# Performance work log

Measured on AMD Instinct MI355X. Metric: run time of the kernel, lower is better.

The kernel has to match this reference:

```python
import jax, jax.numpy as jnp
import numpy as np

B, D, E, K, H, C = 8192, 1024, 8, 2, 2048, 512
LN_EPS = 1e-5


def setup_inputs() -> dict:
    key = jax.random.key(0)
    ks = jax.random.split(key, 6)
    s = 0.02
    return {
        "x": jax.random.normal(ks[0], (B, D), dtype=jnp.float32),
        "Wr": jax.random.normal(ks[1], (E, D), dtype=jnp.float32) * s,  # router weight [E,D]
        "br": jnp.zeros((E,), dtype=jnp.float32),
        "gamma": jnp.ones((E, D), dtype=jnp.float32),   # per-expert LayerNorm scale
        "beta": jnp.zeros((E, D), dtype=jnp.float32),   # per-expert LayerNorm shift
        "W1": jax.random.normal(ks[2], (E, H, D), dtype=jnp.float32) * s,
        "b1": jnp.zeros((E, H), dtype=jnp.float32),
        "W2": jax.random.normal(ks[3], (E, C, H), dtype=jnp.float32) * s,
        "b2": jnp.zeros((E, C), dtype=jnp.float32),
    }


def reference(x, Wr, br, gamma, beta, W1, b1, W2, b2):
    # Router + top-k gating (softmax over the k selected logits only)
    router_logits = x @ Wr.T + br                       # [B,E]
    topk_vals, topk_idx = jax.lax.top_k(router_logits, K)  # [B,K]
    topk_w = jax.nn.softmax(topk_vals, axis=-1)         # [B,K]
    # Dense gate [B,E]: gate[b,e] = sum_j topk_w[b,j] * (topk_idx[b,j]==e)
    gate = (jax.nn.one_hot(topk_idx, E, dtype=x.dtype) * topk_w[..., None]).sum(axis=1)

    # LayerNorm statistics are expert-independent; affine is per-expert
    mu = x.mean(axis=-1, keepdims=True)
    var = ((x - mu) ** 2).mean(axis=-1, keepdims=True)
    xn = (x - mu) * jax.lax.rsqrt(var + LN_EPS)          # [B,D]

    out = jnp.zeros((x.shape[0], C), dtype=x.dtype)
    for e in range(E):  # small fixed expert count
        xe = xn * gamma[e] + beta[e]                     # [B,D]
        h = jax.nn.gelu(xe @ W1[e].T + b1[e], approximate=False)  # [B,H]
        y = h @ W2[e].T + b2[e]                          # [B,C]
        out = out + gate[:, e:e + 1] * y
    return out
```

## Files before the change

### kernel.cpp

```cpp
#include <hip/hip_runtime.h>
#include <hip/hip_bf16.h>
#include <math.h>

#define B_TOK 8192
#define DDIM 1024
#define NEXP 8
#define HDIM 2048
#define CDIM 512
#define LN_EPS 1e-5f
#define MAXTILES 136
#define MAXROWS (MAXTILES * 128)

typedef __attribute__((ext_vector_type(4))) float f32x4;
typedef __attribute__((ext_vector_type(8))) short bf16x8;

__device__ __forceinline__ unsigned short f2bf(float f) {
  __hip_bfloat16 h = __float2bfloat16(f);
  return *reinterpret_cast<unsigned short*>(&h);
}
__device__ __forceinline__ float bf2f(unsigned short u) {
  unsigned int x = ((unsigned int)u) << 16;
  return *reinterpret_cast<float*>(&x);
}

__device__ __forceinline__ void gload_lds16(const unsigned short* g, unsigned short* l) {
  __builtin_amdgcn_global_load_lds(
      (const __attribute__((address_space(1))) unsigned int*)g,
      (__attribute__((address_space(3))) unsigned int*)l, 16, 0, 0);
}

__global__ __launch_bounds__(256) void router_ln_kernel(
    const float* __restrict__ x, const float* __restrict__ Wr,
    const float* __restrict__ br, int* __restrict__ eidx,
    float* __restrict__ wgt, unsigned short* __restrict__ xn) {
  const int wid = threadIdx.x >> 6;
  const int lane = threadIdx.x & 63;
  const int tok = blockIdx.x * 4 + wid;

  const float4* xr = reinterpret_cast<const float4*>(x + (size_t)tok * DDIM);
  float4 xv[4];
  float sum = 0.f, sumsq = 0.f;
  float dot[NEXP];
#pragma unroll
  for (int e = 0; e < NEXP; ++e) dot[e] = 0.f;

#pragma unroll
  for (int i = 0; i < 4; ++i) {
    const int f = i * 64 + lane;
    float4 v = xr[f];
    xv[i] = v;
    sum += v.x + v.y + v.z + v.w;
    sumsq += v.x * v.x + v.y * v.y + v.z * v.z + v.w * v.w;
#pragma unroll
    for (int e = 0; e < NEXP; ++e) {
      float4 w = reinterpret_cast<const float4*>(Wr + e * DDIM)[f];
      dot[e] += v.x * w.x + v.y * w.y + v.z * w.z + v.w * w.w;
    }
  }
#pragma unroll
  for (int off = 32; off > 0; off >>= 1) {
    sum += __shfl_xor(sum, off);
    sumsq += __shfl_xor(sumsq, off);
#pragma unroll
    for (int e = 0; e < NEXP; ++e) dot[e] += __shfl_xor(dot[e], off);
  }
  const float mu = sum * (1.f / DDIM);
  const float var = sumsq * (1.f / DDIM) - mu * mu;
  const float rs = rsqrtf(var + LN_EPS);

  float lg[NEXP];
#pragma unroll
  for (int e = 0; e < NEXP; ++e) lg[e] = dot[e] + br[e];

  int i1 = 0; float v1 = lg[0];
#pragma unroll
  for (int e = 1; e < NEXP; ++e) { if (lg[e] > v1) { v1 = lg[e]; i1 = e; } }
  int i2 = -1; float v2 = -3.4e38f;
#pragma unroll
  for (int e = 0; e < NEXP; ++e) { if (e != i1 && lg[e] > v2) { v2 = lg[e]; i2 = e; } }

  const float e2 = __expf(v2 - v1);
  const float inv = 1.f / (1.f + e2);
  if (lane == 0) {
    eidx[tok * 2] = i1; eidx[tok * 2 + 1] = i2;
    wgt[tok * 2] = inv; wgt[tok * 2 + 1] = e2 * inv;
  }

  unsigned short* xnr = xn + (size_t)tok * DDIM;
#pragma unroll
  for (int i = 0; i < 4; ++i) {
    const int f = i * 64 + lane;
    float4 v = xv[i];
    ushort4 o;
    o.x = f2bf((v.x - mu) * rs);
    o.y = f2bf((v.y - mu) * rs);
    o.z = f2bf((v.z - mu) * rs);
    o.w = f2bf((v.w - mu) * rs);
    reinterpret_cast<ushort4*>(xnr)[f] = o;
  }
}

__global__ __launch_bounds__(256) void sort_kernel(
    const int* __restrict__ eidx,
    int* __restrict__ tokRow,
    int* __restrict__ slot2row,
    int* __restrict__ tileExp,
    int* __restrict__ nTilesOut) {
  __shared__ int cnt[NEXP], segBase[NEXP], cur[NEXP];
  const int tid = threadIdx.x;
  if (tid < NEXP) { cnt[tid] = 0; cur[tid] = 0; }
  __syncthreads();
  for (int t = tid; t < B_TOK * 2; t += 256)
    atomicAdd(&cnt[eidx[t]], 1);
  __syncthreads();
  if (tid == 0) {
    int c = 0;
    for (int e = 0; e < NEXP; ++e) {
      segBase[e] = c;
      const int nt = (cnt[e] + 127) >> 7;
      for (int t = 0; t < nt; ++t) tileExp[(c >> 7) + t] = e;
      for (int p = c + cnt[e]; p < c + nt * 128; ++p) tokRow[p] = 0;
      c += nt * 128;
    }
    *nTilesOut = c >> 7;
  }
  __syncthreads();
  for (int t = tid; t < B_TOK * 2; t += 256) {
    const int e = eidx[t];
    const int pos = segBase[e] + atomicAdd(&cur[e], 1);
    tokRow[pos] = t >> 1;
    slot2row[t] = pos;
  }
}

__global__ __launch_bounds__(256) void prep_w1_kernel(
    const float* __restrict__ W1, const float* __restrict__ gamma,
    const float* __restrict__ beta, const float* __restrict__ b1,
    unsigned short* __restrict__ W1g, float* __restrict__ c1) {
  const int eh = blockIdx.x;
  const int e = eh >> 11;
  const int tid = threadIdx.x;

  float4 w = reinterpret_cast<const float4*>(W1 + (size_t)eh * DDIM)[tid];
  float4 g = reinterpret_cast<const float4*>(gamma + (size_t)e * DDIM)[tid];
  float4 bt = reinterpret_cast<const float4*>(beta + (size_t)e * DDIM)[tid];

  ushort4 o;
  o.x = f2bf(w.x * g.x); o.y = f2bf(w.y * g.y);
  o.z = f2bf(w.z * g.z); o.w = f2bf(w.w * g.w);
  reinterpret_cast<ushort4*>(W1g + (size_t)eh * DDIM)[tid] = o;

  float p = w.x * bt.x + w.y * bt.y + w.z * bt.z + w.w * bt.w;
#pragma unroll
  for (int off = 32; off > 0; off >>= 1) p += __shfl_xor(p, off);
  __shared__ float red[4];
  const int lane = tid & 63, wv = tid >> 6;
  if (lane == 0) red[wv] = p;
  __syncthreads();
  if (tid == 0) c1[eh] = b1[eh] + red[0] + red[1] + red[2] + red[3];
}

__global__ __launch_bounds__(256) void prep_w2_kernel(
    const float* __restrict__ W2, unsigned short* __restrict__ W2b) {
  const int idx = blockIdx.x * 256 + threadIdx.x;
  float4 w = reinterpret_cast<const float4*>(W2)[idx];
  ushort4 o;
  o.x = f2bf(w.x); o.y = f2bf(w.y); o.z = f2bf(w.z); o.w = f2bf(w.w);
  reinterpret_cast<ushort4*>(W2b)[idx] = o;
}

#define BM 128
#define BN 128
#define BKK 64

__global__ __launch_bounds__(256) void gemm1_gelu_kernel(
    const unsigned short* __restrict__ A,
    const unsigned short* __restrict__ W1g,
    const float* __restrict__ c1,
    const int* __restrict__ tokRow, const int* __restrict__ tileExp,
    const int* __restrict__ nTiles,
    unsigned short* __restrict__ Hout) {
  const int bx = blockIdx.x, by = blockIdx.y;
  if (bx >= *nTiles) return;
  const int e = tileExp[bx];

  __shared__ unsigned short lA[BM * BKK];
  __shared__ unsigned short lB[BN * BKK];
  const int tid = threadIdx.x;
  const int lane = tid & 63;
  const int wid = tid >> 6;
  const int wr = wid >> 1, wc = wid & 1;

  const unsigned short* Bbase = W1g + ((size_t)e * HDIM + (size_t)by * BN) * DDIM;
  const float* bias = c1 + e * HDIM;

  const int r = tid >> 3;
  const int cc = (tid & 7) * 8;
  int aRow[4];
#pragma unroll
  for (int i = 0; i < 4; ++i) aRow[i] = tokRow[bx * BM + i * 32 + r];

  f32x4 acc[4][4];
#pragma unroll
  for (int m = 0; m < 4; ++m)
#pragma unroll
    for (int n = 0; n < 4; ++n)
#pragma unroll
      for (int j = 0; j < 4; ++j) acc[m][n][j] = 0.f;

  for (int k0 = 0; k0 < DDIM; k0 += BKK) {
#pragma unroll
    for (int i = 0; i < 4; ++i)
      gload_lds16(A + (size_t)aRow[i] * DDIM + k0 + cc,
                  &lA[(i * 32 + r) * BKK + cc]);
#pragma unroll
    for (int i = 0; i < 4; ++i)
      gload_lds16(Bbase + (size_t)(i * 32 + r) * DDIM + k0 + cc,
                  &lB[(i * 32 + r) * BKK + cc]);
    __syncthreads();
#pragma unroll
    for (int kk = 0; kk < 2; ++kk) {
      bf16x8 af[4], bfr[4];
      const int kof = kk * 32 + (lane >> 4) * 8;
#pragma unroll
      for (int m = 0; m < 4; ++m)
        af[m] = *reinterpret_cast<const bf16x8*>(
            &lA[(wr * 64 + m * 16 + (lane & 15)) * BKK + kof]);
#pragma unroll
      for (int n = 0; n < 4; ++n)
        bfr[n] = *reinterpret_cast<const bf16x8*>(
            &lB[(wc * 64 + n * 16 + (lane & 15)) * BKK + kof]);
#pragma unroll
      for (int m = 0; m < 4; ++m)
#pragma unroll
        for (int n = 0; n < 4; ++n)
          acc[m][n] = __builtin_amdgcn_mfma_f32_16x16x32_bf16(af[m], bfr[n], acc[m][n], 0, 0, 0);
    }
    __syncthreads();
  }

  const int row0 = bx * BM + wr * 64;
  const int col0 = by * BN + wc * 64;
#pragma unroll
  for (int n = 0; n < 4; ++n) {
    const int col = col0 + n * 16 + (lane & 15);
    const float bv = bias[col];
#pragma unroll
    for (int m = 0; m < 4; ++m) {
#pragma unroll
      for (int j = 0; j < 4; ++j) {
        const int row = row0 + m * 16 + (lane >> 4) * 4 + j;
        const float v = acc[m][n][j] + bv;
        const float gl = 0.5f * v * (1.f + erff(v * 0.70710678118654752f));
        Hout[(size_t)row * HDIM + col] = f2bf(gl);
      }
    }
  }
}

__global__ __launch_bounds__(256) void gemm2_kernel(
    const unsigned short* __restrict__ Hbuf,
    const unsigned short* __restrict__ W2b,
    const int* __restrict__ tileExp, const int* __restrict__ nTiles,
    unsigned short* __restrict__ Y) {
  const int bx = blockIdx.x, by = blockIdx.y;
  if (bx >= *nTiles) return;
  const int e = tileExp[bx];

  __shared__ unsigned short lA[BM * BKK];
  __shared__ unsigned short lB[BN * BKK];
  const int tid = threadIdx.x;
  const int lane = tid & 63;
  const int wid = tid >> 6;
  const int wr = wid >> 1, wc = wid & 1;

  const unsigned short* Abase = Hbuf + (size_t)bx * BM * HDIM;
  const unsigned short* Bbase = W2b + ((size_t)e * CDIM + (size_t)by * BN) * HDIM;

  f32x4 acc[4][4];
#pragma unroll
  for (int m = 0; m < 4; ++m)
#pragma unroll
    for (int n = 0; n < 4; ++n)
#pragma unroll
      for (int j = 0; j < 4; ++j) acc[m][n][j] = 0.f;

  const int r = tid >> 3;
  const int cc = (tid & 7) * 8;

  for (int k0 = 0; k0 < HDIM; k0 += BKK) {
#pragma unroll
    for (int i = 0; i < 4; ++i)
      gload_lds16(Abase + (size_t)(i * 32 + r) * HDIM + k0 + cc,
                  &lA[(i * 32 + r) * BKK + cc]);
#pragma unroll
    for (int i = 0; i < 4; ++i)
      gload_lds16(Bbase + (size_t)(i * 32 + r) * HDIM + k0 + cc,
                  &lB[(i * 32 + r) * BKK + cc]);
    __syncthreads();
#pragma unroll
    for (int kk = 0; kk < 2; ++kk) {
      bf16x8 af[4], bfr[4];
      const int kof = kk * 32 + (lane >> 4) * 8;
#pragma unroll
      for (int m = 0; m < 4; ++m)
        af[m] = *reinterpret_cast<const bf16x8*>(
            &lA[(wr * 64 + m * 16 + (lane & 15)) * BKK + kof]);
#pragma unroll
      for (int n = 0; n < 4; ++n)
        bfr[n] = *reinterpret_cast<const bf16x8*>(
            &lB[(wc * 64 + n * 16 + (lane & 15)) * BKK + kof]);
#pragma unroll
      for (int m = 0; m < 4; ++m)
#pragma unroll
        for (int n = 0; n < 4; ++n)
          acc[m][n] = __builtin_amdgcn_mfma_f32_16x16x32_bf16(af[m], bfr[n], acc[m][n], 0, 0, 0);
    }
    __syncthreads();
  }

  const int row0 = bx * BM + wr * 64;
  const int col0 = by * BN + wc * 64;
#pragma unroll
  for (int m = 0; m < 4; ++m) {
#pragma unroll
    for (int j = 0; j < 4; ++j) {
      const int row = row0 + m * 16 + (lane >> 4) * 4 + j;
#pragma unroll
      for (int n = 0; n < 4; ++n) {
        const int col = col0 + n * 16 + (lane & 15);
        Y[(size_t)row * CDIM + col] = f2bf(acc[m][n][j]);
      }
    }
  }
}

__global__ __launch_bounds__(256) void combine_kernel(
    const unsigned short* __restrict__ Y, const int* __restrict__ slot2row,
    const int* __restrict__ eidx, const float* __restrict__ wgt,
    const float* __restrict__ b2, float* __restrict__ out) {
  const int idx = blockIdx.x * 256 + threadIdx.x;
  const int b = idx >> 7;
  const int c4 = (idx & 127) * 4;
  const int r0 = slot2row[b * 2], r1 = slot2row[b * 2 + 1];
  const int e0 = eidx[b * 2], e1 = eidx[b * 2 + 1];
  const float w0 = wgt[b * 2], w1 = wgt[b * 2 + 1];
  ushort4 y0 = *reinterpret_cast<const ushort4*>(Y + (size_t)r0 * CDIM + c4);
  ushort4 y1 = *reinterpret_cast<const ushort4*>(Y + (size_t)r1 * CDIM + c4);
  float4 bb0 = *reinterpret_cast<const float4*>(b2 + e0 * CDIM + c4);
  float4 bb1 = *reinterpret_cast<const float4*>(b2 + e1 * CDIM + c4);
  float4 o;
  o.x = w0 * (bf2f(y0.x) + bb0.x) + w1 * (bf2f(y1.x) + bb1.x);
  o.y = w0 * (bf2f(y0.y) + bb0.y) + w1 * (bf2f(y1.y) + bb1.y);
  o.z = w0 * (bf2f(y0.z) + bb0.z) + w1 * (bf2f(y1.z) + bb1.z);
  o.w = w0 * (bf2f(y0.w) + bb0.w) + w1 * (bf2f(y1.w) + bb1.w);
  *reinterpret_cast<float4*>(out + (size_t)b * CDIM + c4) = o;
}

extern "C" void kernel_launch(void* const* d_in, const int* in_sizes, int n_in,
                              void* d_out, int out_size, void* d_ws, size_t ws_size,
                              hipStream_t stream) {
  const float* x     = (const float*)d_in[0];
  const float* Wr    = (const float*)d_in[1];
  const float* br    = (const float*)d_in[2];
  const float* gamma = (const float*)d_in[3];
  const float* beta  = (const float*)d_in[4];
  const float* W1    = (const float*)d_in[5];
  const float* b1    = (const float*)d_in[6];
  const float* W2    = (const float*)d_in[7];
  const float* b2    = (const float*)d_in[8];
  float* out = (float*)d_out;

  char* ws = (char*)d_ws;
  unsigned short* xn   = (unsigned short*)(ws);
  unsigned short* hbuf = (unsigned short*)(ws + (size_t)16 * 1048576);
  unsigned short* W1g  = (unsigned short*)(ws + (size_t)84 * 1048576);
  unsigned short* ybuf = (unsigned short*)(ws + (size_t)84 * 1048576);
  unsigned short* W2b  = (unsigned short*)(ws + (size_t)116 * 1048576);
  char* misc           = ws + (size_t)132 * 1048576;
  float* c1      = (float*)(misc);
  int* eidx      = (int*)(misc + 65536);
  float* wgt     = (float*)(misc + 2 * 65536);
  int* slot2row  = (int*)(misc + 3 * 65536);
  int* tokRow    = (int*)(misc + 4 * 65536);
  int* tileExp   = (int*)(misc + 4 * 65536 + 69632);
  int* nTiles    = tileExp + MAXTILES;

  router_ln_kernel<<<dim3(B_TOK / 4), dim3(256), 0, stream>>>(x, Wr, br, eidx, wgt, xn);
  sort_kernel<<<dim3(1), dim3(256), 0, stream>>>(eidx, tokRow, slot2row, tileExp, nTiles);
  prep_w1_kernel<<<dim3(NEXP * HDIM), dim3(256), 0, stream>>>(W1, gamma, beta, b1, W1g, c1);
  prep_w2_kernel<<<dim3((NEXP * CDIM * HDIM / 4) / 256), dim3(256), 0, stream>>>(W2, W2b);

  gemm1_gelu_kernel<<<dim3(MAXTILES, HDIM / BN), dim3(256), 0, stream>>>(
      xn, W1g, c1, tokRow, tileExp, nTiles, hbuf);
  gemm2_kernel<<<dim3(MAXTILES, CDIM / BN), dim3(256), 0, stream>>>(
      hbuf, W2b, tileExp, nTiles, ybuf);
  combine_kernel<<<dim3(B_TOK * CDIM / 4 / 256), dim3(256), 0, stream>>>(
      ybuf, slot2row, eidx, wgt, b2, out);
}
```

Before: 315.4 us.

## Rewrite grouped GEMM1 as 256x256 double-buffered 8-wave kernel with swizzled LDS

Replaces the 128x128 single-buffered GEMM1 with a 512-thread, 256x256-tile kernel. It double-buffers global-to-LDS loads and issues the next stage while MFMAs run, using explicit waitcnt/barrier phases, setprio and an XOR-swizzled LDS layout to avoid bank conflicts. Expert segments are padded to 256 rows, and GEMM2 indexing is adapted to the new tiles. The sort kernel switches to wave-ballot aggregated atomics with parallel padding fill, and W2b reuses the xn buffer after GEMM1. Larger padding adds wasted rows, and the hand-written synchronization risks subtle ordering bugs.

```diff
diff --git a/kernel.cpp b/kernel.cpp
--- a/kernel.cpp
+++ b/kernel.cpp
@@ -8,8 +8,8 @@
 #define HDIM 2048
 #define CDIM 512
 #define LN_EPS 1e-5f
-#define MAXTILES 136
-#define MAXROWS (MAXTILES * 128)
+#define MAXT256 72
+#define MAXROWS (MAXT256 * 256)
 
 typedef __attribute__((ext_vector_type(4))) float f32x4;
 typedef __attribute__((ext_vector_type(8))) short bf16x8;
@@ -106,28 +106,51 @@
     int* __restrict__ slot2row,
     int* __restrict__ tileExp,
     int* __restrict__ nTilesOut) {
-  __shared__ int cnt[NEXP], segBase[NEXP], cur[NEXP];
+  __shared__ int cnt[NEXP], segBase[NEXP], segEnd[NEXP], cur[NEXP];
   const int tid = threadIdx.x;
+  const int lane = tid & 63;
   if (tid < NEXP) { cnt[tid] = 0; cur[tid] = 0; }
   __syncthreads();
-  for (int t = tid; t < B_TOK * 2; t += 256)
-    atomicAdd(&cnt[eidx[t]], 1);
+  for (int t = tid; t < B_TOK * 2; t += 256) {
+    const int e = eidx[t];
+#pragma unroll
+    for (int k = 0; k < NEXP; ++k) {
+      unsigned long long m = __ballot(e == k);
+      if (m && lane == 0) atomicAdd(&cnt[k], __popcll(m));
+    }
+  }
   __syncthreads();
   if (tid == 0) {
     int c = 0;
     for (int e = 0; e < NEXP; ++e) {
       segBase[e] = c;
-      const int nt = (cnt[e] + 127) >> 7;
-      for (int t = 0; t < nt; ++t) tileExp[(c >> 7) + t] = e;
-      for (int p = c + cnt[e]; p < c + nt * 128; ++p) tokRow[p] = 0;
-      c += nt * 128;
-    }
-    *nTilesOut = c >> 7;
+      const int nt = (cnt[e] + 255) >> 8;
+      for (int t = 0; t < nt; ++t) tileExp[(c >> 8) + t] = e;
+      c += nt * 256;
+      segEnd[e] = c;
+    }
+    *nTilesOut = c >> 8;
   }
   __syncthreads();
+  for (int e = 0; e < NEXP; ++e) {
+    const int lo = segBase[e] + cnt[e], hi = segEnd[e];
+    for (int p = lo + tid; p < hi; p += 256) tokRow[p] = 0;
+  }
   for (int t = tid; t < B_TOK * 2; t += 256) {
     const int e = eidx[t];
-    const int pos = segBase[e] + atomicAdd(&cur[e], 1);
+    int pos = 0;
+#pragma unroll
+    for (int k = 0; k < NEXP; ++k) {
+      unsigned long long m = __ballot(e == k);
+      if (m) {
+        const int leader = __ffsll((unsigned long long)m) - 1;
+        int base = 0;
+        if (lane == leader) base = atomicAdd(&cur[k], (int)__popcll(m));
+        base = __shfl(base, leader);
+        if (e == k)
+          pos = segBase[k] + base + (int)__popcll(m & ((1ULL << lane) - 1ULL));
+      }
+    }
     tokRow[pos] = t >> 1;
     slot2row[t] = pos;
   }
@@ -169,11 +192,38 @@
   reinterpret_cast<ushort4*>(W2b)[idx] = o;
 }
 
-#define BM 128
-#define BN 128
-#define BKK 64
-
-__global__ __launch_bounds__(256) void gemm1_gelu_kernel(
+template <int QM, int QN>
+__device__ __forceinline__ void phase16(
+    const unsigned short* ldsA, const unsigned short* ldsB,
+    int wm, int wn, int l15, int l4, int l7, f32x4 (&acc)[8][4]) {
+  bf16x8 af[4][2], bfr[2][2];
+#pragma unroll
+  for (int mm = 0; mm < 4; ++mm)
+#pragma unroll
+    for (int ks = 0; ks < 2; ++ks)
+      af[mm][ks] = *reinterpret_cast<const bf16x8*>(
+          &ldsA[(wm * 128 + QM * 64 + mm * 16 + l15) * 64 + ((ks * 4 + l4) ^ l7) * 8]);
+#pragma unroll
+  for (int nn = 0; nn < 2; ++nn)
+#pragma unroll
+    for (int ks = 0; ks < 2; ++ks)
+      bfr[nn][ks] = *reinterpret_cast<const bf16x8*>(
+          &ldsB[(wn * 64 + QN * 32 + nn * 16 + l15) * 64 + ((ks * 4 + l4) ^ l7) * 8]);
+  asm volatile("s_barrier" ::: "memory");
+  __builtin_amdgcn_s_setprio(1);
+#pragma unroll
+  for (int ks = 0; ks < 2; ++ks)
+#pragma unroll
+    for (int mm = 0; mm < 4; ++mm)
+#pragma unroll
+      for (int nn = 0; nn < 2; ++nn)
+        acc[QM * 4 + mm][QN * 2 + nn] = __builtin_amdgcn_mfma_f32_16x16x32_bf16(
+            af[mm][ks], bfr[nn][ks], acc[QM * 4 + mm][QN * 2 + nn], 0, 0, 0);
+  __builtin_amdgcn_s_setprio(0);
+  asm volatile("s_barrier" ::: "memory");
+}
+
+__global__ __launch_bounds__(512, 2) void gemm1_8p_kernel(
     const unsigned short* __restrict__ A,
     const unsigned short* __restrict__ W1g,
     const float* __restrict__ c1,
@@ -184,79 +234,97 @@
   if (bx >= *nTiles) return;
   const int e = tileExp[bx];
 
-  __shared__ unsigned short lA[BM * BKK];
-  __shared__ unsigned short lB[BN * BKK];
+  __shared__ unsigned short lds[2][2][256 * 64];
+
   const int tid = threadIdx.x;
   const int lane = tid & 63;
   const int wid = tid >> 6;
-  const int wr = wid >> 1, wc = wid & 1;
-
-  const unsigned short* Bbase = W1g + ((size_t)e * HDIM + (size_t)by * BN) * DDIM;
-  const float* bias = c1 + e * HDIM;
-
-  const int r = tid >> 3;
-  const int cc = (tid & 7) * 8;
-  int aRow[4];
-#pragma unroll
-  for (int i = 0; i < 4; ++i) aRow[i] = tokRow[bx * BM + i * 32 + r];
-
-  f32x4 acc[4][4];
-#pragma unroll
-  for (int m = 0; m < 4; ++m)
+  const int wm = wid >> 2;
+  const int wn = wid & 3;
+  const int l15 = lane & 15, l4 = lane >> 4, l7 = lane & 7;
+
+  const unsigned short* Bg = W1g + ((size_t)e * HDIM + (size_t)by * 256) * DDIM;
+
+  int tr[4];
+#pragma unroll
+  for (int i = 0; i < 4; ++i) tr[i] = tokRow[bx * 256 + i * 64 + (tid >> 3)];
+  const int sl8 = ((tid & 7) ^ ((tid >> 3) & 7)) * 8;
+
+  f32x4 acc[8][4];
+#pragma unroll
+  for (int m = 0; m < 8; ++m)
 #pragma unroll
     for (int n = 0; n < 4; ++n)
 #pragma unroll
       for (int j = 0; j < 4; ++j) acc[m][n][j] = 0.f;
 
-  for (int k0 = 0; k0 < DDIM; k0 += BKK) {
-#pragma unroll
-    for (int i = 0; i < 4; ++i)
-      gload_lds16(A + (size_t)aRow[i] * DDIM + k0 + cc,
-                  &lA[(i * 32 + r) * BKK + cc]);
-#pragma unroll
-    for (int i = 0; i < 4; ++i)
-      gload_lds16(Bbase + (size_t)(i * 32 + r) * DDIM + k0 + cc,
-                  &lB[(i * 32 + r) * BKK + cc]);
-    __syncthreads();
-#pragma unroll
-    for (int kk = 0; kk < 2; ++kk) {
-      bf16x8 af[4], bfr[4];
-      const int kof = kk * 32 + (lane >> 4) * 8;
-#pragma unroll
-      for (int m = 0; m < 4; ++m)
-        af[m] = *reinterpret_cast<const bf16x8*>(
-            &lA[(wr * 64 + m * 16 + (lane & 15)) * BKK + kof]);
-#pragma unroll
-      for (int n = 0; n < 4; ++n)
-        bfr[n] = *reinterpret_cast<const bf16x8*>(
-            &lB[(wc * 64 + n * 16 + (lane & 15)) * BKK + kof]);
-#pragma unroll
-      for (int m = 0; m < 4; ++m)
-#pragma unroll
-        for (int n = 0; n < 4; ++n)
-          acc[m][n] = __builtin_amdgcn_mfma_f32_16x16x32_bf16(af[m], bfr[n], acc[m][n], 0, 0, 0);
-    }
-    __syncthreads();
-  }
-
-  const int row0 = bx * BM + wr * 64;
-  const int col0 = by * BN + wc * 64;
-#pragma unroll
-  for (int n = 0; n < 4; ++n) {
-    const int col = col0 + n * 16 + (lane & 15);
-    const float bv = bias[col];
-#pragma unroll
-    for (int m = 0; m < 4; ++m) {
+  auto stage8 = [&](int b, int k0) {
+#pragma unroll
+    for (int h = 0; h < 2; ++h)
+#pragma unroll
+      for (int q = 0; q < 2; ++q)
+        gload_lds16(A + (size_t)tr[h * 2 + q] * DDIM + k0 + sl8,
+                    &lds[b][0][h * 8192 + q * 4096 + tid * 8]);
+#pragma unroll
+    for (int h = 0; h < 2; ++h)
+#pragma unroll
+      for (int q = 0; q < 2; ++q)
+        gload_lds16(Bg + (size_t)(h * 128 + q * 64 + (tid >> 3)) * DDIM + k0 + sl8,
+                    &lds[b][1][h * 8192 + q * 4096 + tid * 8]);
+  };
+
+  stage8(0, 0);
+  stage8(1, 64);
+
+  int cur = 0;
+#pragma unroll 1
+  for (int kt = 0; kt < 15; ++kt) {
+    asm volatile("s_waitcnt vmcnt(8)" ::: "memory");
+    __builtin_amdgcn_sched_barrier(0);
+    asm volatile("s_barrier" ::: "memory");
+    const unsigned short* ldsA = lds[cur][0];
+    const unsigned short* ldsB = lds[cur][1];
+    phase16<0, 0>(ldsA, ldsB, wm, wn, l15, l4, l7, acc);
+    phase16<0, 1>(ldsA, ldsB, wm, wn, l15, l4, l7, acc);
+    phase16<1, 0>(ldsA, ldsB, wm, wn, l15, l4, l7, acc);
+    phase16<1, 1>(ldsA, ldsB, wm, wn, l15, l4, l7, acc);
+    if (kt < 14) stage8(cur, (kt + 2) * 64);
+    cur ^= 1;
+  }
+  asm volatile("s_waitcnt vmcnt(0)" ::: "memory");
+  __builtin_amdgcn_sched_barrier(0);
+  asm volatile("s_barrier" ::: "memory");
+  {
+    const unsigned short* ldsA = lds[cur][0];
+    const unsigned short* ldsB = lds[cur][1];
+    phase16<0, 0>(ldsA, ldsB, wm, wn, l15, l4, l7, acc);
+    phase16<0, 1>(ldsA, ldsB, wm, wn, l15, l4, l7, acc);
+    phase16<1, 0>(ldsA, ldsB, wm, wn, l15, l4, l7, acc);
+    phase16<1, 1>(ldsA, ldsB, wm, wn, l15, l4, l7, acc);
+  }
+
+  const float* biasp = c1 + e * HDIM + by * 256 + wn * 64;
+  unsigned short* Hbase = Hout + (size_t)(bx * 256 + wm * 128) * HDIM + by * 256 + wn * 64;
+#pragma unroll
+  for (int m = 0; m < 8; ++m) {
+#pragma unroll
+    for (int n = 0; n < 4; ++n) {
+      const int col = n * 16 + l15;
+      const float bv = biasp[col];
 #pragma unroll
       for (int j = 0; j < 4; ++j) {
-        const int row = row0 + m * 16 + (lane >> 4) * 4 + j;
+        const int row = m * 16 + l4 * 4 + j;
         const float v = acc[m][n][j] + bv;
         const float gl = 0.5f * v * (1.f + erff(v * 0.70710678118654752f));
-        Hout[(size_t)row * HDIM + col] = f2bf(gl);
+        Hbase[(size_t)row * HDIM + col] = f2bf(gl);
       }
     }
   }
 }
+
+#define BM 128
+#define BN 128
+#define BKK 64
 
 __global__ __launch_bounds__(256) void gemm2_kernel(
     const unsigned short* __restrict__ Hbuf,
@@ -264,8 +332,8 @@
     const int* __restrict__ tileExp, const int* __restrict__ nTiles,
     unsigned short* __restrict__ Y) {
   const int bx = blockIdx.x, by = blockIdx.y;
-  if (bx >= *nTiles) return;
-  const int e = tileExp[bx];
+  if ((bx >> 1) >= *nTiles) return;
+  const int e = tileExp[bx >> 1];
 
   __shared__ unsigned short lA[BM * BKK];
   __shared__ unsigned short lB[BN * BKK];
@@ -373,27 +441,29 @@
 
   char* ws = (char*)d_ws;
   unsigned short* xn   = (unsigned short*)(ws);
+  unsigned short* W2b  = (unsigned short*)(ws);
   unsigned short* hbuf = (unsigned short*)(ws + (size_t)16 * 1048576);
-  unsigned short* W1g  = (unsigned short*)(ws + (size_t)84 * 1048576);
-  unsigned short* ybuf = (unsigned short*)(ws + (size_t)84 * 1048576);
-  unsigned short* W2b  = (unsigned short*)(ws + (size_t)116 * 1048576);
-  char* misc           = ws + (size_t)132 * 1048576;
+  unsigned short* W1g  = (unsigned short*)(ws + (size_t)88 * 1048576);
+  unsigned short* ybuf = (unsigned short*)(ws + (size_t)88 * 1048576);
+  char* misc           = ws + (size_t)120 * 1048576;
   float* c1      = (float*)(misc);
   int* eidx      = (int*)(misc + 65536);
   float* wgt     = (float*)(misc + 2 * 65536);
   int* slot2row  = (int*)(misc + 3 * 65536);
   int* tokRow    = (int*)(misc + 4 * 65536);
-  int* tileExp   = (int*)(misc + 4 * 65536 + 69632);
-  int* nTiles    = tileExp + MAXTILES;
+  int* tileExp   = (int*)(misc + 4 * 65536 + 131072);
+  int* nTiles    = tileExp + MAXT256;
 
   router_ln_kernel<<<dim3(B_TOK / 4), dim3(256), 0, stream>>>(x, Wr, br, eidx, wgt, xn);
   sort_kernel<<<dim3(1), dim3(256), 0, stream>>>(eidx, tokRow, slot2row, tileExp, nTiles);
   prep_w1_kernel<<<dim3(NEXP * HDIM), dim3(256), 0, stream>>>(W1, gamma, beta, b1, W1g, c1);
+
+  gemm1_8p_kernel<<<dim3(MAXT256, HDIM / 256), dim3(512), 0, stream>>>(
+      xn, W1g, c1, tokRow, tileExp, nTiles, hbuf);
+
   prep_w2_kernel<<<dim3((NEXP * CDIM * HDIM / 4) / 256), dim3(256), 0, stream>>>(W2, W2b);
 
-  gemm1_gelu_kernel<<<dim3(MAXTILES, HDIM / BN), dim3(256), 0, stream>>>(
-      xn, W1g, c1, tokRow, tileExp, nTiles, hbuf);
-  gemm2_kernel<<<dim3(MAXTILES, CDIM / BN), dim3(256), 0, stream>>>(
+  gemm2_kernel<<<dim3(MAXT256 * 2, CDIM / BN), dim3(256), 0, stream>>>(
       hbuf, W2b, tileExp, nTiles, ybuf);
   combine_kernel<<<dim3(B_TOK * CDIM / 4 / 256), dim3(256), 0, stream>>>(
       ybuf, slot2row, eidx, wgt, b2, out);
```

After: 411.6 us. 1.3x slower.

## Swizzle LDS tiles, remap grid for XCD locality, pad experts to 256 rows

Applied to the files above, without the earlier changes.

Adds an XOR swizzle to the LDS layout of A and B tiles in both GEMMs so the MFMA fragment reads avoid bank conflicts. Flattens the grid and remaps block indices so that blocks sharing the same weight or activation tiles land on the same XCD (blockIdx & 7), aiming for better L2 reuse. Pads expert segments to 256 rows so each expert covers whole pairs of 128-row tiles. Reorders the workspace so W2b reuses the xn region and is converted after GEMM1. The coarser padding adds more wasted rows per expert.

```diff
diff --git a/kernel.cpp b/kernel.cpp
--- a/kernel.cpp
+++ b/kernel.cpp
@@ -8,8 +8,8 @@
 #define HDIM 2048
 #define CDIM 512
 #define LN_EPS 1e-5f
-#define MAXTILES 136
-#define MAXROWS (MAXTILES * 128)
+#define MAXT256 72
+#define MAXROWS (MAXT256 * 256)
 
 typedef __attribute__((ext_vector_type(4))) float f32x4;
 typedef __attribute__((ext_vector_type(8))) short bf16x8;
@@ -117,12 +117,12 @@
     int c = 0;
     for (int e = 0; e < NEXP; ++e) {
       segBase[e] = c;
-      const int nt = (cnt[e] + 127) >> 7;
-      for (int t = 0; t < nt; ++t) tileExp[(c >> 7) + t] = e;
-      for (int p = c + cnt[e]; p < c + nt * 128; ++p) tokRow[p] = 0;
-      c += nt * 128;
-    }
-    *nTilesOut = c >> 7;
+      const int nt = (cnt[e] + 255) >> 8;
+      for (int t = 0; t < nt; ++t) tileExp[(c >> 8) + t] = e;
+      for (int p = c + cnt[e]; p < c + nt * 256; ++p) tokRow[p] = 0;
+      c += nt * 256;
+    }
+    *nTilesOut = c >> 8;
   }
   __syncthreads();
   for (int t = tid; t < B_TOK * 2; t += 256) {
@@ -180,9 +180,13 @@
     const int* __restrict__ tokRow, const int* __restrict__ tileExp,
     const int* __restrict__ nTiles,
     unsigned short* __restrict__ Hout) {
-  const int bx = blockIdx.x, by = blockIdx.y;
-  if (bx >= *nTiles) return;
-  const int e = tileExp[bx];
+  const int flat = blockIdx.x;
+  const int p = flat & 7;
+  const int q = flat >> 3;
+  const int by = p * 2 + (q / 144);
+  const int bx = q % 144;
+  if ((bx >> 1) >= *nTiles) return;
+  const int e = tileExp[bx >> 1];
 
   __shared__ unsigned short lA[BM * BKK];
   __shared__ unsigned short lB[BN * BKK];
@@ -190,12 +194,13 @@
   const int lane = tid & 63;
   const int wid = tid >> 6;
   const int wr = wid >> 1, wc = wid & 1;
+  const int l15 = lane & 15, l4 = lane >> 4;
 
   const unsigned short* Bbase = W1g + ((size_t)e * HDIM + (size_t)by * BN) * DDIM;
-  const float* bias = c1 + e * HDIM;
 
   const int r = tid >> 3;
-  const int cc = (tid & 7) * 8;
+  const int swz = ((tid & 7) ^ (r & 7)) * 8;
+  const int dst = (tid & 7) * 8;
   int aRow[4];
 #pragma unroll
   for (int i = 0; i < 4; ++i) aRow[i] = tokRow[bx * BM + i * 32 + r];
@@ -211,25 +216,25 @@
   for (int k0 = 0; k0 < DDIM; k0 += BKK) {
 #pragma unroll
     for (int i = 0; i < 4; ++i)
-      gload_lds16(A + (size_t)aRow[i] * DDIM + k0 + cc,
-                  &lA[(i * 32 + r) * BKK + cc]);
+      gload_lds16(A + (size_t)aRow[i] * DDIM + k0 + swz,
+                  &lA[(i * 32 + r) * BKK + dst]);
 #pragma unroll
     for (int i = 0; i < 4; ++i)
-      gload_lds16(Bbase + (size_t)(i * 32 + r) * DDIM + k0 + cc,
-                  &lB[(i * 32 + r) * BKK + cc]);
+      gload_lds16(Bbase + (size_t)(i * 32 + r) * DDIM + k0 + swz,
+                  &lB[(i * 32 + r) * BKK + dst]);
     __syncthreads();
 #pragma unroll
     for (int kk = 0; kk < 2; ++kk) {
       bf16x8 af[4], bfr[4];
-      const int kof = kk * 32 + (lane >> 4) * 8;
+      const int slot = (((kk * 4 + l4) ^ (l15 & 7)) * 8);
 #pragma unroll
       for (int m = 0; m < 4; ++m)
         af[m] = *reinterpret_cast<const bf16x8*>(
-            &lA[(wr * 64 + m * 16 + (lane & 15)) * BKK + kof]);
+            &lA[(wr * 64 + m * 16 + l15) * BKK + slot]);
 #pragma unroll
       for (int n = 0; n < 4; ++n)
         bfr[n] = *reinterpret_cast<const bf16x8*>(
-            &lB[(wc * 64 + n * 16 + (lane & 15)) * BKK + kof]);
+            &lB[(wc * 64 + n * 16 + l15) * BKK + slot]);
 #pragma unroll
       for (int m = 0; m < 4; ++m)
 #pragma unroll
@@ -241,15 +246,16 @@
 
   const int row0 = bx * BM + wr * 64;
   const int col0 = by * BN + wc * 64;
+  const float* bias = c1 + e * HDIM;
 #pragma unroll
   for (int n = 0; n < 4; ++n) {
-    const int col = col0 + n * 16 + (lane & 15);
+    const int col = col0 + n * 16 + l15;
     const float bv = bias[col];
 #pragma unroll
     for (int m = 0; m < 4; ++m) {
 #pragma unroll
       for (int j = 0; j < 4; ++j) {
-        const int row = row0 + m * 16 + (lane >> 4) * 4 + j;
+        const int row = row0 + m * 16 + l4 * 4 + j;
         const float v = acc[m][n][j] + bv;
         const float gl = 0.5f * v * (1.f + erff(v * 0.70710678118654752f));
         Hout[(size_t)row * HDIM + col] = f2bf(gl);
@@ -263,9 +269,13 @@
     const unsigned short* __restrict__ W2b,
     const int* __restrict__ tileExp, const int* __restrict__ nTiles,
     unsigned short* __restrict__ Y) {
-  const int bx = blockIdx.x, by = blockIdx.y;
-  if (bx >= *nTiles) return;
-  const int e = tileExp[bx];
+  const int flat = blockIdx.x;
+  const int p = flat & 7;
+  const int q = flat >> 3;
+  const int by = p >> 1;
+  const int bx = (p & 1) * 72 + q;
+  if ((bx >> 1) >= *nTiles) return;
+  const int e = tileExp[bx >> 1];
 
   __shared__ unsigned short lA[BM * BKK];
   __shared__ unsigned short lB[BN * BKK];
@@ -273,6 +283,7 @@
   const int lane = tid & 63;
   const int wid = tid >> 6;
   const int wr = wid >> 1, wc = wid & 1;
+  const int l15 = lane & 15, l4 = lane >> 4;
 
   const unsigned short* Abase = Hbuf + (size_t)bx * BM * HDIM;
   const unsigned short* Bbase = W2b + ((size_t)e * CDIM + (size_t)by * BN) * HDIM;
@@ -286,30 +297,31 @@
       for (int j = 0; j < 4; ++j) acc[m][n][j] = 0.f;
 
   const int r = tid >> 3;
-  const int cc = (tid & 7) * 8;
+  const int swz = ((tid & 7) ^ (r & 7)) * 8;
+  const int dst = (tid & 7) * 8;
 
   for (int k0 = 0; k0 < HDIM; k0 += BKK) {
 #pragma unroll
     for (int i = 0; i < 4; ++i)
-      gload_lds16(Abase + (size_t)(i * 32 + r) * HDIM + k0 + cc,
-                  &lA[(i * 32 + r) * BKK + cc]);
+      gload_lds16(Abase + (size_t)(i * 32 + r) * HDIM + k0 + swz,
+                  &lA[(i * 32 + r) * BKK + dst]);
 #pragma unroll
     for (int i = 0; i < 4; ++i)
-      gload_lds16(Bbase + (size_t)(i * 32 + r) * HDIM + k0 + cc,
-                  &lB[(i * 32 + r) * BKK + cc]);
+      gload_lds16(Bbase + (size_t)(i * 32 + r) * HDIM + k0 + swz,
+                  &lB[(i * 32 + r) * BKK + dst]);
     __syncthreads();
 #pragma unroll
     for (int kk = 0; kk < 2; ++kk) {
       bf16x8 af[4], bfr[4];
-      const int kof = kk * 32 + (lane >> 4) * 8;
+      const int slot = (((kk * 4 + l4) ^ (l15 & 7)) * 8);
 #pragma unroll
       for (int m = 0; m < 4; ++m)
         af[m] = *reinterpret_cast<const bf16x8*>(
-            &lA[(wr * 64 + m * 16 + (lane & 15)) * BKK + kof]);
+            &lA[(wr * 64 + m * 16 + l15) * BKK + slot]);
 #pragma unroll
       for (int n = 0; n < 4; ++n)
         bfr[n] = *reinterpret_cast<const bf16x8*>(
-            &lB[(wc * 64 + n * 16 + (lane & 15)) * BKK + kof]);
+            &lB[(wc * 64 + n * 16 + l15) * BKK + slot]);
 #pragma unroll
       for (int m = 0; m < 4; ++m)
 #pragma unroll
@@ -325,10 +337,10 @@
   for (int m = 0; m < 4; ++m) {
 #pragma unroll
     for (int j = 0; j < 4; ++j) {
-      const int row = row0 + m * 16 + (lane >> 4) * 4 + j;
+      const int row = row0 + m * 16 + l4 * 4 + j;
 #pragma unroll
       for (int n = 0; n < 4; ++n) {
-        const int col = col0 + n * 16 + (lane & 15);
+        const int col = col0 + n * 16 + l15;
         Y[(size_t)row * CDIM + col] = f2bf(acc[m][n][j]);
       }
     }
@@ -373,27 +385,29 @@
 
   char* ws = (char*)d_ws;
   unsigned short* xn   = (unsigned short*)(ws);
+  unsigned short* W2b  = (unsigned short*)(ws);
   unsigned short* hbuf = (unsigned short*)(ws + (size_t)16 * 1048576);
-  unsigned short* W1g  = (unsigned short*)(ws + (size_t)84 * 1048576);
-  unsigned short* ybuf = (unsigned short*)(ws + (size_t)84 * 1048576);
-  unsigned short* W2b  = (unsigned short*)(ws + (size_t)116 * 1048576);
-  char* misc           = ws + (size_t)132 * 1048576;
+  unsigned short* W1g  = (unsigned short*)(ws + (size_t)88 * 1048576);
+  unsigned short* ybuf = (unsigned short*)(ws + (size_t)88 * 1048576);
+  char* misc           = ws + (size_t)120 * 1048576;
   float* c1      = (float*)(misc);
   int* eidx      = (int*)(misc + 65536);
   float* wgt     = (float*)(misc + 2 * 65536);
   int* slot2row  = (int*)(misc + 3 * 65536);
   int* tokRow    = (int*)(misc + 4 * 65536);
-  int* tileExp   = (int*)(misc + 4 * 65536 + 69632);
-  int* nTiles    = tileExp + MAXTILES;
+  int* tileExp   = (int*)(misc + 4 * 65536 + 131072);
+  int* nTiles    = tileExp + MAXT256;
 
   router_ln_kernel<<<dim3(B_TOK / 4), dim3(256), 0, stream>>>(x, Wr, br, eidx, wgt, xn);
   sort_kernel<<<dim3(1), dim3(256), 0, stream>>>(eidx, tokRow, slot2row, tileExp, nTiles);
   prep_w1_kernel<<<dim3(NEXP * HDIM), dim3(256), 0, stream>>>(W1, gamma, beta, b1, W1g, c1);
+
+  gemm1_gelu_kernel<<<dim3(2304), dim3(256), 0, stream>>>(
+      xn, W1g, c1, tokRow, tileExp, nTiles, hbuf);
+
   prep_w2_kernel<<<dim3((NEXP * CDIM * HDIM / 4) / 256), dim3(256), 0, stream>>>(W2, W2b);
 
-  gemm1_gelu_kernel<<<dim3(MAXTILES, HDIM / BN), dim3(256), 0, stream>>>(
-      xn, W1g, c1, tokRow, tileExp, nTiles, hbuf);
-  gemm2_kernel<<<dim3(MAXTILES, CDIM / BN), dim3(256), 0, stream>>>(
+  gemm2_kernel<<<dim3(576), dim3(256), 0, stream>>>(
       hbuf, W2b, tileExp, nTiles, ybuf);
   combine_kernel<<<dim3(B_TOK * CDIM / 4 / 256), dim3(256), 0, stream>>>(
       ybuf, slot2row, eidx, wgt, b2, out);
```

Result: faster. 296.5 us (-6.0%).
